# Performance work log

Measured on AMD Instinct MI355X. Metric: run time of the kernel, lower is better.

The kernel has to match this reference:

```python
import jax, jax.numpy as jnp
import numpy as np


def _cdist(a, b):
    # a: [B, N, D], b: [B, M, D] -> [B, N, M] Euclidean distances
    sq = (jnp.sum(a * a, -1)[:, :, None]
          + jnp.sum(b * b, -1)[:, None, :]
          - 2.0 * jnp.einsum('bnd,bmd->bnm', a, b))
    return jnp.sqrt(jnp.maximum(sq, 1e-12))


def setup_inputs() -> dict:
    key = jax.random.key(0)
    k1, k2, k3, k4 = jax.random.split(key, 4)
    B, N, NC, S = 2, 32768, 1024, 32
    centers = jax.random.normal(k1, (B, NC, 3), dtype=jnp.float32)
    radius = jax.random.uniform(k2, (B, NC, 1), dtype=jnp.float32)
    xyz = jax.random.normal(k3, (B, N, 3), dtype=jnp.float32)
    sphere_points = jax.random.normal(k4, (B, NC * S, 3), dtype=jnp.float32)
    return {"centers": centers, "radius": radius, "xyz": xyz,
            "sphere_points": sphere_points}


def reference(centers, radius, xyz, sphere_points):
    B, NC, _ = centers.shape
    # point -> center distances  [B, N, NC]
    dmat = _cdist(xyz, centers)
    cd_p_to_c = jnp.min(dmat, axis=-1)            # [B, N]
    idx_p_to_c = jnp.argmin(dmat, axis=-1)        # [B, N]
    # gather radius of nearest center for each point
    radius_from_p = jnp.take_along_axis(radius[..., 0], idx_p_to_c, axis=1)  # [B, N]
    # is_surface=False branch: clamp positive diffs to 0, then mean(|.|)
    diff = jnp.minimum(radius_from_p - cd_p_to_c, 0.0)
    radius_difference_p_to_c = jnp.mean(jnp.abs(diff), axis=1)               # [B]
    # sphere-point -> sample distances  [B, N, NC*S]
    dmat_sp = _cdist(xyz, sphere_points)
    cd_sp_to_p = jnp.min(dmat_sp, axis=1)          # [B, NC*S]
    max_cd_sp_to_p = jnp.max(cd_sp_to_p.reshape(B, NC, -1), axis=-1)         # [B, NC]
    radius_difference_c_to_p = jnp.mean(jnp.abs(max_cd_sp_to_p), axis=1)     # [B]
    res = radius_difference_c_to_p + radius_difference_p_to_c
    return jnp.mean(res)  # reduction='mean'
```

## Files before the change

kernel.cpp:

```cpp
#include <hip/hip_runtime.h>

#define B   2
#define N   32768
#define NC  1024
#define S   32
#define NSP (NC * S)

#define CHUNK 512
#define NCH   (N / CHUNK)
#define BLKT  256
#define FR    4
#define COLS_BLK (4 * FR * 32)
#define GRIDX (NSP / COLS_BLK)
#define P2C_BLOCKS (B * N / 256)
#define SP2P_BLOCKS (GRIDX * NCH * B)

typedef __attribute__((ext_vector_type(8)))  short short8v;
typedef __attribute__((ext_vector_type(16))) float f32x16;
typedef const __attribute__((address_space(1))) void gvoid_t;
typedef __attribute__((address_space(3))) void svoid_t;

static __device__ __forceinline__ unsigned short f2b(float x) {
    unsigned u = __float_as_uint(x);
    return (unsigned short)((u + 0x7FFFu + ((u >> 16) & 1u)) >> 16);
}
static __device__ __forceinline__ float b2f(unsigned short u) {
    return __uint_as_float(((unsigned)u) << 16);
}
static __device__ __forceinline__ float min3f(float a, float b, float c) {
    return fminf(fminf(a, b), c);
}


__global__ __launch_bounds__(256) void k_prep(const float* __restrict__ xyz,
                                              unsigned short* __restrict__ Afrag,
                                              unsigned* __restrict__ minsq,
                                              unsigned* __restrict__ accw) {
    int i = blockIdx.x * 256 + threadIdx.x;
    if (i < 2) accw[i] = 0u;
    minsq[i] = 0x7F800000u;

    const float* q = xyz + (size_t)i * 3;
    float qx = q[0], qy = q[1], qz = q[2];
    float h = 0.5f * (qx * qx + qy * qy + qz * qz);
    unsigned short xh = f2b(-qx), yh = f2b(-qy), zh = f2b(-qz);
    unsigned short xl = f2b(-qx - b2f(xh));
    unsigned short yl = f2b(-qy - b2f(yh));
    unsigned short zl = f2b(-qz - b2f(zh));
    unsigned short hh = f2b(h), hl = f2b(h - b2f(hh));

    int b = i >> 15, j = i & (N - 1);
    int tile = j >> 5, r = j & 31;
    unsigned short* base = Afrag + ((size_t)b * N + (size_t)tile * 32) * 16;
    uint4 s0, s1;
    s0.x = (unsigned)xh | ((unsigned)yh << 16);
    s0.y = (unsigned)zh | ((unsigned)xl << 16);
    s0.z = (unsigned)yl | ((unsigned)zl << 16);
    s0.w = (unsigned)xh | ((unsigned)yh << 16);
    s1.x = (unsigned)zh | ((unsigned)hh << 16);
    s1.y = (unsigned)hl;
    s1.z = 0u; s1.w = 0u;
    *(uint4*)(base + (size_t)r * 8)        = s0;
    *(uint4*)(base + (size_t)(r + 32) * 8) = s1;
}

__global__ __launch_bounds__(BLKT) void k_main(const float* __restrict__ centers,
                                               const float* __restrict__ radius,
                                               const float* __restrict__ xyz,
                                               const float* __restrict__ sp,
                                               const unsigned short* __restrict__ Afrag,
                                               unsigned* __restrict__ minsq,
                                               float* __restrict__ acc) {
    __shared__ union {
        unsigned short afr[CHUNK * 16];
        struct { float4 c4[NC]; float rad[NC]; } pc;
    } sm;
    const int tid = threadIdx.x, wid = tid >> 6, lane = tid & 63;

    if (blockIdx.x < P2C_BLOCKS) {
        const int g = blockIdx.x * 256 + tid;
        const int b = g >> 15;
        const float* cb = centers + (size_t)b * NC * 3;
        for (int t4 = tid; t4 < NC / 4; t4 += 256) {
            float4 f0 = ((const float4*)cb)[t4 * 3 + 0];
            float4 f1 = ((const float4*)cb)[t4 * 3 + 1];
            float4 f2 = ((const float4*)cb)[t4 * 3 + 2];
            float x0 = f0.x, y0 = f0.y, z0 = f0.z;
            float x1 = f0.w, y1 = f1.x, z1 = f1.y;
            float x2 = f1.z, y2 = f1.w, z2 = f2.x;
            float x3 = f2.y, y3 = f2.z, z3 = f2.w;
            sm.pc.c4[t4 * 4 + 0] = make_float4(x0, y0, z0, 0.5f * (x0 * x0 + y0 * y0 + z0 * z0));
            sm.pc.c4[t4 * 4 + 1] = make_float4(x1, y1, z1, 0.5f * (x1 * x1 + y1 * y1 + z1 * z1));
            sm.pc.c4[t4 * 4 + 2] = make_float4(x2, y2, z2, 0.5f * (x2 * x2 + y2 * y2 + z2 * z2));
            sm.pc.c4[t4 * 4 + 3] = make_float4(x3, y3, z3, 0.5f * (x3 * x3 + y3 * y3 + z3 * z3));
        }
        {
            const float* rb = radius + (size_t)b * NC;
            float4 r4 = ((const float4*)rb)[tid];
            sm.pc.rad[tid * 4 + 0] = r4.x; sm.pc.rad[tid * 4 + 1] = r4.y;
            sm.pc.rad[tid * 4 + 2] = r4.z; sm.pc.rad[tid * 4 + 3] = r4.w;
        }
        __syncthreads();

        const float* p = xyz + (size_t)g * 3;
        const float px = p[0], py = p[1], pz = p[2];
        const float pp = px * px + py * py + pz * pz;
        float tmin = 1e30f;
        int   imin = 0;
        #pragma unroll 4
        for (int c = 0; c < NC; ++c) {
            float4 q = sm.pc.c4[c];
            float  t = q.w - px * q.x - py * q.y - pz * q.z;
            if (t < tmin) { tmin = t; imin = c; }
        }
        const float cd = sqrtf(fmaxf(2.0f * tmin + pp, 1e-12f));
        float contrib = fmaxf(cd - sm.pc.rad[imin], 0.0f) * (1.0f / N);
        #pragma unroll
        for (int o = 32; o > 0; o >>= 1) contrib += __shfl_down(contrib, o);
        __shared__ float wsum[4];
        if (lane == 0) wsum[wid] = contrib;
        __syncthreads();
        if (tid == 0) atomicAdd(acc, wsum[0] + wsum[1] + wsum[2] + wsum[3]);
        return;
    }

    const int sbid  = blockIdx.x - P2C_BLOCKS;
    const int ct    = sbid & (GRIDX - 1);
    const int chunk = (sbid >> 6) & (NCH - 1);
    const int b     = sbid >> 12;

    const char* src = (const char*)(Afrag +
                        ((size_t)b * N + (size_t)chunk * CHUNK) * 16);
    #pragma unroll
    for (int it = 0; it < 4; ++it) {
        int off = it * 4096 + wid * 1024;
        __builtin_amdgcn_global_load_lds((gvoid_t*)(src + off + lane * 16),
                                         (svoid_t*)((char*)sm.afr + off), 16, 0, 0);
    }

    const int colbase = ct * COLS_BLK + wid * (FR * 32) + (lane & 31);
    float pp[FR]; short8v bf[FR];
    #pragma unroll
    for (int f = 0; f < FR; ++f) {
        const float* p = sp + ((size_t)b * NSP + colbase + f * 32) * 3;
        float qx = p[0], qy = p[1], qz = p[2];
        pp[f] = qx * qx + qy * qy + qz * qz;
        unsigned short xh = f2b(qx), yh = f2b(qy), zh = f2b(qz);
        unsigned short xl = f2b(qx - b2f(xh));
        unsigned short yl = f2b(qy - b2f(yh));
        unsigned short zl = f2b(qz - b2f(zh));
        short8v v;
        if (lane < 32) {
            v[0] = (short)xh; v[1] = (short)yh; v[2] = (short)zh;
            v[3] = (short)xh; v[4] = (short)yh; v[5] = (short)zh;
            v[6] = (short)xl; v[7] = (short)yl;
        } else {
            v[0] = (short)zl; v[1] = (short)0x3F80; v[2] = (short)0x3F80;
            v[3] = 0; v[4] = 0; v[5] = 0; v[6] = 0; v[7] = 0;
        }
        bf[f] = v;
    }
    f32x16 zero;
    #pragma unroll
    for (int i = 0; i < 16; ++i) zero[i] = 0.0f;

    float run[FR];
    #pragma unroll
    for (int f = 0; f < FR; ++f) run[f] = 1e30f;

    __syncthreads();

    const unsigned short* ap = sm.afr + lane * 8;
    #pragma unroll 2
    for (int t = 0; t < CHUNK / 32; ++t) {
        short8v a = *(const short8v*)(ap + (size_t)t * 512);
        #pragma unroll
        for (int f = 0; f < FR; ++f) {
            f32x16 d = __builtin_amdgcn_mfma_f32_32x32x16_bf16(a, bf[f], zero, 0, 0, 0);
            float r0 = min3f(d[0],  d[1],  d[2]);
            float r1 = min3f(d[3],  d[4],  d[5]);
            float r2 = min3f(d[6],  d[7],  d[8]);
            float r3 = min3f(d[9],  d[10], d[11]);
            float r4 = min3f(d[12], d[13], d[14]);
            float r5 = min3f(r0, r1, d[15]);
            float r6 = min3f(r2, r3, r4);
            run[f] = min3f(run[f], r5, r6);
        }
    }

    #pragma unroll
    for (int f = 0; f < FR; ++f)
        run[f] = fminf(run[f], __shfl_xor(run[f], 32, 64));
    if (lane < 32) {
        unsigned* mb = minsq + (size_t)b * NSP + colbase;
        #pragma unroll
        for (int f = 0; f < FR; ++f) {
            float sq = fmaxf(2.0f * run[f] + pp[f], 0.0f);
            atomicMin(mb + f * 32, __float_as_uint(sq));
        }
    }
}

__global__ __launch_bounds__(256) void k_fin(const unsigned* __restrict__ minsq,
                                             float* __restrict__ acc,
                                             unsigned* __restrict__ counter,
                                             float* __restrict__ out) {
    const int tid = threadIdx.x;
    const int i = blockIdx.x * 256 + tid;
    float cd = sqrtf(fmaxf(__uint_as_float(minsq[i]), 1e-12f));
    #pragma unroll
    for (int o = 16; o > 0; o >>= 1) cd = fmaxf(cd, __shfl_xor(cd, o, 64));

    float contrib = ((tid & 31) == 0) ? cd * (1.0f / NC) : 0.0f;
    #pragma unroll
    for (int o = 32; o > 0; o >>= 1) contrib += __shfl_down(contrib, o);
    __shared__ float wsum[4];
    if ((tid & 63) == 0) wsum[tid >> 6] = contrib;
    __syncthreads();
    if (tid == 0) atomicAdd(acc, wsum[0] + wsum[1] + wsum[2] + wsum[3]);

    __shared__ int lastf;
    if (tid == 0) {
        __threadfence();
        unsigned old = atomicAdd(counter, 1u);
        lastf = (old == (unsigned)(gridDim.x - 1));
    }
    __syncthreads();
    if (lastf && tid == 0)
        out[0] = atomicAdd(acc, 0.0f) * (1.0f / B);
}

extern "C" void kernel_launch(void* const* d_in, const int* in_sizes, int n_in,
                              void* d_out, int out_size, void* d_ws, size_t ws_size,
                              hipStream_t stream) {
    const float* centers = (const float*)d_in[0];
    const float* radius  = (const float*)d_in[1];
    const float* xyz     = (const float*)d_in[2];
    const float* sp      = (const float*)d_in[3];
    float* out = (float*)d_out;

    unsigned short* Afrag = (unsigned short*)d_ws;
    unsigned* minsq  = (unsigned*)((char*)d_ws + (size_t)B * N * 32);
    float*    acc    = (float*)((char*)minsq + (size_t)B * NSP * 4);
    unsigned* counter = (unsigned*)acc + 1;

    hipLaunchKernelGGL(k_prep, dim3(B * N / 256), dim3(256), 0, stream,
                       xyz, Afrag, minsq, (unsigned*)acc);
    hipLaunchKernelGGL(k_main, dim3(P2C_BLOCKS + SP2P_BLOCKS), dim3(BLKT), 0, stream,
                       centers, radius, xyz, sp, Afrag, minsq, acc);
    hipLaunchKernelGGL(k_fin, dim3(B * NSP / 256), dim3(256), 0, stream,
                       minsq, acc, counter, out);
}
```

Baseline: 162.9 us.

## Fuse point-fragment prep into main kernel and replace prep with memsets

Removes the separate k_prep kernel and its global bf16 split-fragment buffer. Each sphere-point block now reads its chunk of xyz directly, builds the hi/lo bf16 fragments in registers and writes them to LDS. Initialization of minsq and the accumulator moves to hipMemsetAsync, and launch bounds add a minimum occupancy hint. The aim is to cut a kernel launch and a global write/read round trip, at the cost of recomputing the conversion redundantly in every column block and losing the async global-to-LDS load.

New measurement: 169.7 us. +4.2%, slower.

```diff
diff --git a/kernel.cpp b/kernel.cpp
--- a/kernel.cpp
+++ b/kernel.cpp
@@ -17,8 +17,6 @@
 
 typedef __attribute__((ext_vector_type(8)))  short short8v;
 typedef __attribute__((ext_vector_type(16))) float f32x16;
-typedef const __attribute__((address_space(1))) void gvoid_t;
-typedef __attribute__((address_space(3))) void svoid_t;
 
 static __device__ __forceinline__ unsigned short f2b(float x) {
     unsigned u = __float_as_uint(x);
@@ -32,45 +30,13 @@
 }
 
 
-__global__ __launch_bounds__(256) void k_prep(const float* __restrict__ xyz,
-                                              unsigned short* __restrict__ Afrag,
-                                              unsigned* __restrict__ minsq,
-                                              unsigned* __restrict__ accw) {
-    int i = blockIdx.x * 256 + threadIdx.x;
-    if (i < 2) accw[i] = 0u;
-    minsq[i] = 0x7F800000u;
-
-    const float* q = xyz + (size_t)i * 3;
-    float qx = q[0], qy = q[1], qz = q[2];
-    float h = 0.5f * (qx * qx + qy * qy + qz * qz);
-    unsigned short xh = f2b(-qx), yh = f2b(-qy), zh = f2b(-qz);
-    unsigned short xl = f2b(-qx - b2f(xh));
-    unsigned short yl = f2b(-qy - b2f(yh));
-    unsigned short zl = f2b(-qz - b2f(zh));
-    unsigned short hh = f2b(h), hl = f2b(h - b2f(hh));
-
-    int b = i >> 15, j = i & (N - 1);
-    int tile = j >> 5, r = j & 31;
-    unsigned short* base = Afrag + ((size_t)b * N + (size_t)tile * 32) * 16;
-    uint4 s0, s1;
-    s0.x = (unsigned)xh | ((unsigned)yh << 16);
-    s0.y = (unsigned)zh | ((unsigned)xl << 16);
-    s0.z = (unsigned)yl | ((unsigned)zl << 16);
-    s0.w = (unsigned)xh | ((unsigned)yh << 16);
-    s1.x = (unsigned)zh | ((unsigned)hh << 16);
-    s1.y = (unsigned)hl;
-    s1.z = 0u; s1.w = 0u;
-    *(uint4*)(base + (size_t)r * 8)        = s0;
-    *(uint4*)(base + (size_t)(r + 32) * 8) = s1;
-}
-
-__global__ __launch_bounds__(BLKT) void k_main(const float* __restrict__ centers,
-                                               const float* __restrict__ radius,
-                                               const float* __restrict__ xyz,
-                                               const float* __restrict__ sp,
-                                               const unsigned short* __restrict__ Afrag,
-                                               unsigned* __restrict__ minsq,
-                                               float* __restrict__ acc) {
+__global__ __launch_bounds__(BLKT, 8)
+void k_main(const float* __restrict__ centers,
+            const float* __restrict__ radius,
+            const float* __restrict__ xyz,
+            const float* __restrict__ sp,
+            unsigned* __restrict__ minsq,
+            float* __restrict__ acc) {
     __shared__ union {
         unsigned short afr[CHUNK * 16];
         struct { float4 c4[NC]; float rad[NC]; } pc;
@@ -129,13 +95,29 @@
     const int chunk = (sbid >> 6) & (NCH - 1);
     const int b     = sbid >> 12;
 
-    const char* src = (const char*)(Afrag +
-                        ((size_t)b * N + (size_t)chunk * CHUNK) * 16);
-    #pragma unroll
-    for (int it = 0; it < 4; ++it) {
-        int off = it * 4096 + wid * 1024;
-        __builtin_amdgcn_global_load_lds((gvoid_t*)(src + off + lane * 16),
-                                         (svoid_t*)((char*)sm.afr + off), 16, 0, 0);
+    const float* xb = xyz + ((size_t)b * N + (size_t)chunk * CHUNK) * 3;
+    #pragma unroll
+    for (int rr = 0; rr < CHUNK / BLKT; ++rr) {
+        const int r = rr * BLKT + tid;
+        float qx = xb[r * 3 + 0], qy = xb[r * 3 + 1], qz = xb[r * 3 + 2];
+        float h = 0.5f * (qx * qx + qy * qy + qz * qz);
+        unsigned short xh = f2b(-qx), yh = f2b(-qy), zh = f2b(-qz);
+        unsigned short xl = f2b(-qx - b2f(xh));
+        unsigned short yl = f2b(-qy - b2f(yh));
+        unsigned short zl = f2b(-qz - b2f(zh));
+        unsigned short hh = f2b(h), hl = f2b(h - b2f(hh));
+        uint4 s0, s1;
+        s0.x = (unsigned)xh | ((unsigned)yh << 16);
+        s0.y = (unsigned)zh | ((unsigned)xl << 16);
+        s0.z = (unsigned)yl | ((unsigned)zl << 16);
+        s0.w = (unsigned)xh | ((unsigned)yh << 16);
+        s1.x = (unsigned)zh | ((unsigned)hh << 16);
+        s1.y = (unsigned)hl;
+        s1.z = 0u; s1.w = 0u;
+        const int tile = r >> 5, rw = r & 31;
+        uint4* dst = (uint4*)sm.afr;
+        dst[tile * 64 + rw]      = s0;
+        dst[tile * 64 + 32 + rw] = s1;
     }
 
     const int colbase = ct * COLS_BLK + wid * (FR * 32) + (lane & 31);
@@ -239,15 +221,15 @@
     const float* sp      = (const float*)d_in[3];
     float* out = (float*)d_out;
 
-    unsigned short* Afrag = (unsigned short*)d_ws;
-    unsigned* minsq  = (unsigned*)((char*)d_ws + (size_t)B * N * 32);
-    float*    acc    = (float*)((char*)minsq + (size_t)B * NSP * 4);
+    unsigned* minsq   = (unsigned*)d_ws;
+    float*    acc     = (float*)((char*)d_ws + (size_t)B * NSP * 4);
     unsigned* counter = (unsigned*)acc + 1;
 
-    hipLaunchKernelGGL(k_prep, dim3(B * N / 256), dim3(256), 0, stream,
-                       xyz, Afrag, minsq, (unsigned*)acc);
+    hipMemsetAsync(minsq, 0x7F, (size_t)B * NSP * 4, stream);
+    hipMemsetAsync(acc, 0, 8, stream);
+
     hipLaunchKernelGGL(k_main, dim3(P2C_BLOCKS + SP2P_BLOCKS), dim3(BLKT), 0, stream,
-                       centers, radius, xyz, sp, Afrag, minsq, acc);
+                       centers, radius, xyz, sp, minsq, acc);
     hipLaunchKernelGGL(k_fin, dim3(B * NSP / 256), dim3(256), 0, stream,
                        minsq, acc, counter, out);
 }
```
